# Kernel tuning notes

Measured on AMD Instinct MI355X. Metric: run time of the kernel, lower is better.

The kernel has to match this reference:

```python
import jax, jax.numpy as jnp
import numpy as np

N = 100000      # nodes
E = 800000      # edges (avg degree 8)
F = 5           # num_node_features
D = 128         # embed_dim
H = 4           # heads
HD = D // H     # per-head dim = 32
H1, H2 = 64, 128  # mlp hidden dims


def _mlp(x, W1, b1, W2, b2, W3, b3):
    h = jax.nn.relu(x @ W1 + b1)
    h = jax.nn.relu(h @ W2 + b2)
    return h @ W3 + b3


def setup_inputs() -> dict:
    key = jax.random.key(0)
    ks = jax.random.split(key, 24)
    g = lambda i, shape: (jax.random.normal(ks[i], shape, dtype=jnp.float32) * 0.05)
    z = lambda d: jnp.zeros((d,), dtype=jnp.float32)
    return {
        "x": jax.random.normal(ks[0], (N, F), dtype=jnp.float32),
        "edge_index": jax.random.randint(ks[1], (2, E), 0, N),
        # mlp_prep: F -> 64 -> 128 -> D
        "prep_W1": g(2, (F, H1)),  "prep_b1": z(H1),
        "prep_W2": g(3, (H1, H2)), "prep_b2": z(H2),
        "prep_W3": g(4, (H2, D)),  "prep_b3": z(D),
        # mlp_update: D -> 64 -> 128 -> D
        "upd_W1": g(5, (D, H1)),   "upd_b1": z(H1),
        "upd_W2": g(6, (H1, H2)),  "upd_b2": z(H2),
        "upd_W3": g(7, (H2, D)),   "upd_b3": z(D),
        # TransformerConv projections (heads=4, per-head 32, concat -> D)
        "q_W": g(8, (D, D)),  "q_b": z(D),
        "k_W": g(9, (D, D)),  "k_b": z(D),
        "v_W": g(10, (D, D)), "v_b": z(D),
        "skip_W": g(11, (D, D)), "skip_b": z(D),
    }


def _transformer_conv(x, edge_index, q_W, q_b, k_W, k_b, v_W, v_b, skip_W, skip_b):
    # PyG TransformerConv: messages flow src=edge_index[0] -> dst=edge_index[1]
    src, dst = edge_index[0], edge_index[1]
    q = (x @ q_W + q_b).reshape(N, H, HD)
    k = (x @ k_W + k_b).reshape(N, H, HD)
    v = (x @ v_W + v_b).reshape(N, H, HD)
    scale = 1.0 / np.sqrt(HD).astype(np.float32)
    # per-edge attention logits [E, H]
    score = jnp.einsum('ehd,ehd->eh', q[dst], k[src]) * scale
    # segment softmax over incoming edges of each destination node
    m = jax.ops.segment_max(score, dst, num_segments=N)          # [N, H]
    e = jnp.exp(score - m[dst])                                  # [E, H]
    denom = jax.ops.segment_sum(e, dst, num_segments=N)         # [N, H]
    alpha = e / denom[dst]                                       # [E, H]
    # scatter-aggregate weighted values
    agg = jax.ops.segment_sum(alpha[..., None] * v[src], dst, num_segments=N)  # [N, H, HD]
    return agg.reshape(N, H * HD) + (x @ skip_W + skip_b)


def reference(x, edge_index,
              prep_W1, prep_b1, prep_W2, prep_b2, prep_W3, prep_b3,
              upd_W1, upd_b1, upd_W2, upd_b2, upd_W3, upd_b3,
              q_W, q_b, k_W, k_b, v_W, v_b, skip_W, skip_b):
    h_init = _mlp(x, prep_W1, prep_b1, prep_W2, prep_b2, prep_W3, prep_b3)
    h = _transformer_conv(h_init, edge_index, q_W, q_b, k_W, k_b, v_W, v_b, skip_W, skip_b)
    return h + _mlp(h, upd_W1, upd_b1, upd_W2, upd_b2, upd_W3, upd_b3)
```

## Files before the change

kernel.cpp:

```cpp
#include <hip/hip_runtime.h>
#include <hip/hip_bf16.h>

#define N_  100000
#define F_  5
#define D_  128
#define H_  4
#define HD_ 32
#define E_  800000

typedef __attribute__((ext_vector_type(8))) short bf16x8;
typedef __attribute__((ext_vector_type(4))) float f32x4;

__device__ __forceinline__ unsigned short f2bf(float f) {
  unsigned u = __float_as_uint(f);
  u += 0x7FFF + ((u >> 16) & 1);
  return (unsigned short)(u >> 16);
}

__device__ __forceinline__ unsigned pk2(float a, float b) {
  __hip_bfloat162 h = __float22bfloat162_rn(make_float2(a, b));
  return *(unsigned*)&h;
}

__device__ __forceinline__ float2 bf2f2(unsigned u) {
  float2 r;
  r.x = __uint_as_float(u << 16);
  r.y = __uint_as_float(u & 0xffff0000u);
  return r;
}

__device__ __forceinline__ float rowsum8(float x) {
  x += __int_as_float(__builtin_amdgcn_update_dpp(0, __float_as_int(x), 0x0B1, 0xF, 0xF, false));
  x += __int_as_float(__builtin_amdgcn_update_dpp(0, __float_as_int(x), 0x04E, 0xF, 0xF, false));
  x += __int_as_float(__builtin_amdgcn_update_dpp(0, __float_as_int(x), 0x141, 0xF, 0xF, false));
  return x;
}

template<int K, int M>
__device__ __forceinline__ void wconv_one(const float* __restrict__ W,
                                          unsigned short* __restrict__ WT,
                                          int idx) {
  const int r = idx & 7;
  const int l = (idx >> 3) & 15;
  const int rest = idx >> 7;
  const int kq = rest % (K / 8);
  const int i  = rest / (K / 8);
  WT[idx] = f2bf(W[(kq * 8 + r) * M + i * 16 + l]);
}

#define WCONV_NB 480
#define SCAN_NB ((N_ + 255) / 256)

__global__ __launch_bounds__(256) void k_wconv_all(
    const float* __restrict__ w0, const float* __restrict__ w1,
    const float* __restrict__ w2, const float* __restrict__ w3,
    const float* __restrict__ w4, const float* __restrict__ w5,
    const float* __restrict__ w6, const float* __restrict__ w7,
    const float* __restrict__ w8, unsigned short* __restrict__ WT,
    int* __restrict__ deg)
{
  if (blockIdx.x >= WCONV_NB) {
    const int i = (blockIdx.x - WCONV_NB) * 256 + threadIdx.x;
    if (i < N_) deg[i] = 0;
    return;
  }
  const int idx = blockIdx.x * 256 + threadIdx.x;
  if (idx < 8192)        wconv_one<64, 128>(w0, WT,          idx);
  else if (idx < 24576)  wconv_one<128,128>(w1, WT + 8192,   idx - 8192);
  else if (idx < 40960)  wconv_one<128,128>(w2, WT + 24576,  idx - 24576);
  else if (idx < 57344)  wconv_one<128,128>(w3, WT + 40960,  idx - 40960);
  else if (idx < 73728)  wconv_one<128,128>(w4, WT + 57344,  idx - 57344);
  else if (idx < 90112)  wconv_one<128,128>(w5, WT + 73728,  idx - 73728);
  else if (idx < 98304)  wconv_one<128, 64>(w6, WT + 90112,  idx - 90112);
  else if (idx < 106496) wconv_one<64, 128>(w7, WT + 98304,  idx - 98304);
  else                   wconv_one<128,128>(w8, WT + 106496, idx - 106496);
}

template<int K, int M>
__device__ __forceinline__ void gemm_frag64(const unsigned short* sX,
                                            const unsigned short* __restrict__ WT,
                                            f32x4 (*acc)[4],
                                            int wr, int l16, int kg)
{
  constexpr int SX = K + 8;
  constexpr int IF = M / 64;
  #pragma unroll
  for (int i = 0; i < IF; ++i)
    #pragma unroll
    for (int j = 0; j < 4; ++j) acc[i][j] = (f32x4){0.f, 0.f, 0.f, 0.f};
  #pragma unroll
  for (int k0 = 0; k0 < K; k0 += 32) {
    const int kq = k0 / 8 + kg;
    bf16x8 aw[IF];
    #pragma unroll
    for (int i = 0; i < IF; ++i)
      aw[i] = *(const bf16x8*)&WT[(((wr * IF + i) * (K / 8) + kq) * 16 + l16) * 8];
    #pragma unroll
    for (int j = 0; j < 4; ++j) {
      const bf16x8 bx = *(const bf16x8*)&sX[(j * 16 + l16) * SX + k0 + kg * 8];
      #pragma unroll
      for (int i = 0; i < IF; ++i)
        acc[i][j] = __builtin_amdgcn_mfma_f32_16x16x32_bf16(aw[i], bx, acc[i][j], 0, 0, 0);
    }
  }
}

template<int M, bool RELU, int SXO>
__device__ __forceinline__ void acc_to_lds64(unsigned short* sY, f32x4 (*acc)[4],
                                             const float* __restrict__ bias,
                                             int wr, int l16, int kg)
{
  constexpr int IF = M / 64;
  float4 b4[IF];
  #pragma unroll
  for (int i = 0; i < IF; ++i)
    b4[i] = *(const float4*)&bias[(wr * IF + i) * 16 + kg * 4];
  #pragma unroll
  for (int j = 0; j < 4; ++j) {
    const int row = j * 16 + l16;
    #pragma unroll
    for (int i = 0; i < IF; ++i) {
      const int f0 = (wr * IF + i) * 16 + kg * 4;
      float ox = acc[i][j][0] + b4[i].x, oy = acc[i][j][1] + b4[i].y;
      float oz = acc[i][j][2] + b4[i].z, ow = acc[i][j][3] + b4[i].w;
      if constexpr (RELU) {
        ox = fmaxf(ox, 0.f); oy = fmaxf(oy, 0.f);
        oz = fmaxf(oz, 0.f); ow = fmaxf(ow, 0.f);
      }
      uint2 p;
      p.x = pk2(ox, oy);
      p.y = pk2(oz, ow);
      *(uint2*)&sY[row * SXO + f0] = p;
    }
  }
}

__global__ __launch_bounds__(256) void k_prep_proj(
    const float* __restrict__ x,
    const float* __restrict__ pW1, const float* __restrict__ pb1,
    const unsigned short* __restrict__ wt_p2, const float* __restrict__ pb2,
    const unsigned short* __restrict__ wt_p3, const float* __restrict__ pb3,
    const unsigned short* __restrict__ wt_q, const float* __restrict__ qb,
    const unsigned short* __restrict__ wt_k, const float* __restrict__ kb,
    const unsigned short* __restrict__ wt_v, const float* __restrict__ vb,
    const unsigned short* __restrict__ wt_s, const float* __restrict__ sb,
    unsigned short* __restrict__ q16, unsigned short* __restrict__ k16,
    unsigned short* __restrict__ v16, float* __restrict__ out)
{
  __shared__ __align__(16) unsigned short bufA[64 * 72];
  __shared__ __align__(16) unsigned short bufB[64 * 136];

  const int t = threadIdx.x;
  const int node0 = blockIdx.x * 64;
  const int lane = t & 63;
  const int wr = t >> 6;
  const int l16 = lane & 15, kg = lane >> 4;

  float* sxs = (float*)bufB;
  float* sw1 = (float*)bufB + 320;
  {
    const long gbase = (long)node0 * F_;
    for (int i = t; i < 64 * F_; i += 256) {
      const long g = gbase + i;
      sxs[i] = (g < (long)N_ * F_) ? x[g] : 0.f;
    }
    for (int i = t; i < 384; i += 256)
      sw1[i] = (i < 320) ? pW1[i] : pb1[i - 320];
  }
  __syncthreads();

  {
    const int n = t >> 2;
    const int f0b = (t & 3) * 16;
    float xr[F_];
    #pragma unroll
    for (int k = 0; k < F_; ++k) xr[k] = sxs[n * F_ + k];
    const float* sb1 = sw1 + 320;
    #pragma unroll
    for (int q = 0; q < 4; ++q) {
      float o[4];
      #pragma unroll
      for (int jj = 0; jj < 4; ++jj) {
        const int f = f0b + q * 4 + jj;
        float a = sb1[f];
        #pragma unroll
        for (int k = 0; k < F_; ++k) a = fmaf(xr[k], sw1[k * 64 + f], a);
        o[jj] = fmaxf(a, 0.f);
      }
      uint2 pkd;
      pkd.x = pk2(o[0], o[1]);
      pkd.y = pk2(o[2], o[3]);
      *(uint2*)&bufA[n * 72 + f0b + q * 4] = pkd;
    }
  }
  __syncthreads();

  f32x4 acc[2][4];

  gemm_frag64<64, 128>(bufA, wt_p2, acc, wr, l16, kg);
  acc_to_lds64<128, true, 136>(bufB, acc, pb2, wr, l16, kg);
  __syncthreads();

  gemm_frag64<128, 128>(bufB, wt_p3, acc, wr, l16, kg);
  __syncthreads();
  acc_to_lds64<128, false, 136>(bufB, acc, pb3, wr, l16, kg);
  __syncthreads();

  {
    const unsigned short* wtsP[3] = {wt_q, wt_k, wt_v};
    const float* bsP[3] = {qb, kb, vb};
    unsigned short* ysP[3] = {q16, k16, v16};
    #pragma unroll
    for (int ws = 0; ws < 3; ++ws) {
      gemm_frag64<128, 128>(bufB, wtsP[ws], acc, wr, l16, kg);
      const float* __restrict__ bias = bsP[ws];
      unsigned short* __restrict__ Yb = ysP[ws];
      float4 b4[2];
      #pragma unroll
      for (int i = 0; i < 2; ++i)
        b4[i] = *(const float4*)&bias[(wr * 2 + i) * 16 + kg * 4];
      #pragma unroll
      for (int j = 0; j < 4; ++j) {
        const int node = node0 + j * 16 + l16;
        if (node >= N_) continue;
        #pragma unroll
        for (int i = 0; i < 2; ++i) {
          const int f0 = (wr * 2 + i) * 16 + kg * 4;
          uint2 ob;
          ob.x = pk2(acc[i][j][0] + b4[i].x, acc[i][j][1] + b4[i].y);
          ob.y = pk2(acc[i][j][2] + b4[i].z, acc[i][j][3] + b4[i].w);
          *(uint2*)&Yb[(long)node * D_ + f0] = ob;
        }
      }
    }
  }

  gemm_frag64<128, 128>(bufB, wt_s, acc, wr, l16, kg);
  {
    float4 b4[2];
    #pragma unroll
    for (int i = 0; i < 2; ++i)
      b4[i] = *(const float4*)&sb[(wr * 2 + i) * 16 + kg * 4];
    #pragma unroll
    for (int j = 0; j < 4; ++j) {
      const int node = node0 + j * 16 + l16;
      if (node >= N_) continue;
      #pragma unroll
      for (int i = 0; i < 2; ++i) {
        const int f0 = (wr * 2 + i) * 16 + kg * 4;
        float4 o = make_float4(acc[i][j][0] + b4[i].x, acc[i][j][1] + b4[i].y,
                               acc[i][j][2] + b4[i].z, acc[i][j][3] + b4[i].w);
        *(float4*)&out[(long)node * D_ + f0] = o;
      }
    }
  }
}

__global__ __launch_bounds__(256) void k_update(
    const unsigned short* __restrict__ wt_u1, const float* __restrict__ ub1,
    const unsigned short* __restrict__ wt_u2, const float* __restrict__ ub2,
    const unsigned short* __restrict__ wt_u3, const float* __restrict__ ub3,
    float* __restrict__ out)
{
  __shared__ __align__(16) unsigned short bufA[64 * 72];
  __shared__ __align__(16) unsigned short bufB[64 * 136];

  const int t = threadIdx.x;
  const int node0 = blockIdx.x * 64;
  const int lane = t & 63;
  const int wr = t >> 6;
  const int l16 = lane & 15, kg = lane >> 4;

  #pragma unroll
  for (int i = 0; i < 8; ++i) {
    const int g = t + 256 * i;
    const int row = g >> 5;
    const int kc  = g & 31;
    const int node = node0 + row;
    float4 xv = (node < N_) ? ((const float4*)out)[(long)node * 32 + kc]
                            : make_float4(0.f, 0.f, 0.f, 0.f);
    uint2 p;
    p.x = pk2(xv.x, xv.y);
    p.y = pk2(xv.z, xv.w);
    *(uint2*)&bufB[row * 136 + kc * 4] = p;
  }
  __syncthreads();

  f32x4 acc[2][4];

  gemm_frag64<128, 64>(bufB, wt_u1, acc, wr, l16, kg);
  acc_to_lds64<64, true, 72>(bufA, acc, ub1, wr, l16, kg);
  __syncthreads();

  gemm_frag64<64, 128>(bufA, wt_u2, acc, wr, l16, kg);
  acc_to_lds64<128, true, 136>(bufB, acc, ub2, wr, l16, kg);
  __syncthreads();

  gemm_frag64<128, 128>(bufB, wt_u3, acc, wr, l16, kg);
  {
    float4 b4[2];
    #pragma unroll
    for (int i = 0; i < 2; ++i)
      b4[i] = *(const float4*)&ub3[(wr * 2 + i) * 16 + kg * 4];
    #pragma unroll
    for (int j = 0; j < 4; ++j) {
      const int node = node0 + j * 16 + l16;
      if (node >= N_) continue;
      #pragma unroll
      for (int i = 0; i < 2; ++i) {
        const int f0 = (wr * 2 + i) * 16 + kg * 4;
        const float4 r = *(const float4*)&out[(long)node * D_ + f0];
        float4 o = make_float4(acc[i][j][0] + b4[i].x + r.x,
                               acc[i][j][1] + b4[i].y + r.y,
                               acc[i][j][2] + b4[i].z + r.z,
                               acc[i][j][3] + b4[i].w + r.w);
        *(float4*)&out[(long)node * D_ + f0] = o;
      }
    }
  }
}

__global__ __launch_bounds__(256) void k_hist(const int* __restrict__ ei,
                                              int* __restrict__ deg) {
  int e = blockIdx.x * 256 + threadIdx.x;
  if (e < E_) atomicAdd(&deg[ei[E_ + e]], 1);
}

__global__ __launch_bounds__(256) void k_scan1(const int* __restrict__ deg,
                                               int* __restrict__ off,
                                               int* __restrict__ bsum) {
  __shared__ int s[256];
  const int t = threadIdx.x;
  const int i = blockIdx.x * 256 + t;
  const int v = (i < N_) ? deg[i] : 0;
  s[t] = v;
  __syncthreads();
  #pragma unroll
  for (int o = 1; o < 256; o <<= 1) {
    int u = (t >= o) ? s[t - o] : 0;
    __syncthreads();
    s[t] += u;
    __syncthreads();
  }
  if (i < N_) off[i] = s[t] - v;
  if (t == 255) bsum[blockIdx.x] = s[255];
}

__global__ __launch_bounds__(256) void k_scan23(const int* __restrict__ off,
                                                const int* __restrict__ bsum,
                                                int* __restrict__ cur,
                                                const int* __restrict__ deg,
                                                int2* __restrict__ meta) {
  __shared__ int sacc[256];
  const int t = threadIdx.x;
  const int bid = blockIdx.x;
  int s = 0;
  for (int j = t; j < bid; j += 256) s += bsum[j];
  sacc[t] = s;
  __syncthreads();
  #pragma unroll
  for (int o = 128; o > 0; o >>= 1) {
    if (t < o) sacc[t] += sacc[t + o];
    __syncthreads();
  }
  const int prefix = sacc[0];
  const int i = bid * 256 + t;
  if (i < N_) {
    const int o = off[i] + prefix;
    cur[i] = o;
    meta[i] = make_int2(o, deg[i]);
  }
}

__global__ __launch_bounds__(256) void k_fill(const int* __restrict__ ei,
                                              int* __restrict__ cur,
                                              int* __restrict__ esrc) {
  int e = blockIdx.x * 256 + threadIdx.x;
  if (e < E_) {
    int src = ei[e], dst = ei[E_ + e];
    int pos = atomicAdd(&cur[dst], 1);
    esrc[pos] = src;
  }
}

__global__ __launch_bounds__(256) void k_attn(
    const int* __restrict__ esrc, const int2* __restrict__ meta,
    const unsigned short* __restrict__ q,
    const unsigned short* __restrict__ kbuf,
    const unsigned short* __restrict__ vbuf,
    float* __restrict__ out)
{
  const int t = threadIdx.x;
  const unsigned node = blockIdx.x * 8 + (t >> 5);
  const int c = t & 31;
  const float C = 0.17677669529663687f * 1.4426950408889634f;

  const int2 md = meta[node];
  const int start = md.x, cnt = md.y;
  const int end = start + cnt;

  const uint2 qu = *(const uint2*)&q[(node << 7) + 4u * c];
  const float2 q01 = bf2f2(qu.x), q23 = bf2f2(qu.y);
  const float qx0 = q01.x * C, qx1 = q01.y * C;
  const float qx2 = q23.x * C, qx3 = q23.y * C;

  float l = 0.f, a0 = 0.f, a1 = 0.f, a2 = 0.f, a3 = 0.f;

  const int P = (cnt + 1) >> 1;
  if (P > 0) {
    bool v1c = (start + 1) < end;
    unsigned i0 = esrc[start];
    unsigned i1 = esrc[v1c ? start + 1 : start];
    uint2 kA = *(const uint2*)&kbuf[(i0 << 7) + 4u * c];
    uint2 kB = *(const uint2*)&kbuf[(i1 << 7) + 4u * c];
    uint2 wA = *(const uint2*)&vbuf[(i0 << 7) + 4u * c];
    uint2 wB = *(const uint2*)&vbuf[(i1 << 7) + 4u * c];
    bool v0n = (start + 2) < end, v1n = (start + 3) < end;
    unsigned i0n = esrc[v0n ? start + 2 : start];
    unsigned i1n = esrc[v1n ? start + 3 : start];

    for (int it = 0;;) {
      const bool more = (it + 1) < P;
      uint2 kAn, kBn, wAn, wBn;
      unsigned i0f = 0, i1f = 0;
      bool v0f = false, v1f = false;
      if (more) {
        kAn = *(const uint2*)&kbuf[(i0n << 7) + 4u * c];
        kBn = *(const uint2*)&kbuf[(i1n << 7) + 4u * c];
        wAn = *(const uint2*)&vbuf[(i0n << 7) + 4u * c];
        wBn = *(const uint2*)&vbuf[(i1n << 7) + 4u * c];
        const int ef = start + 2 * (it + 2);
        v0f = ef < end; v1f = (ef + 1) < end;
        i0f = esrc[v0f ? ef : start];
        i1f = esrc[v1f ? ef + 1 : start];
      }

      const float2 ka01 = bf2f2(kA.x), ka23 = bf2f2(kA.y);
      const float2 kb01 = bf2f2(kB.x), kb23 = bf2f2(kB.y);
      float sA = fmaf(qx0, ka01.x, fmaf(qx1, ka01.y, fmaf(qx2, ka23.x, qx3 * ka23.y)));
      float sB = fmaf(qx0, kb01.x, fmaf(qx1, kb01.y, fmaf(qx2, kb23.x, qx3 * kb23.y)));
      sA = rowsum8(sA);
      sB = rowsum8(sB);
      const float eA = __builtin_amdgcn_exp2f(sA);
      const float eB = v1c ? __builtin_amdgcn_exp2f(sB) : 0.f;
      const float2 va01 = bf2f2(wA.x), va23 = bf2f2(wA.y);
      const float2 vb01 = bf2f2(wB.x), vb23 = bf2f2(wB.y);
      l += eA + eB;
      a0 = fmaf(eA, va01.x, fmaf(eB, vb01.x, a0));
      a1 = fmaf(eA, va01.y, fmaf(eB, vb01.y, a1));
      a2 = fmaf(eA, va23.x, fmaf(eB, vb23.x, a2));
      a3 = fmaf(eA, va23.y, fmaf(eB, vb23.y, a3));

      if (!more) break;
      ++it;
      kA = kAn; kB = kBn; wA = wAn; wB = wBn;
      v1c = v1n;
      v0n = v0f; v1n = v1f;
      i0n = i0f; i1n = i1f;
    }
  }

  if (l > 0.f) {
    const float inv = 1.0f / l;
    float4* op = (float4*)&out[(node << 7) + 4u * c];
    float4 cv = *op;
    cv.x += a0 * inv;
    cv.y += a1 * inv;
    cv.z += a2 * inv;
    cv.w += a3 * inv;
    *op = cv;
  }
}

extern "C" void kernel_launch(void* const* d_in, const int* in_sizes, int n_in,
                              void* d_out, int out_size, void* d_ws, size_t ws_size,
                              hipStream_t stream) {
  const float* x   = (const float*)d_in[0];
  const int*   ei  = (const int*)d_in[1];
  const float* pW1 = (const float*)d_in[2];  const float* pb1 = (const float*)d_in[3];
  const float* pW2 = (const float*)d_in[4];  const float* pb2 = (const float*)d_in[5];
  const float* pW3 = (const float*)d_in[6];  const float* pb3 = (const float*)d_in[7];
  const float* uW1 = (const float*)d_in[8];  const float* ub1 = (const float*)d_in[9];
  const float* uW2 = (const float*)d_in[10]; const float* ub2 = (const float*)d_in[11];
  const float* uW3 = (const float*)d_in[12]; const float* ub3 = (const float*)d_in[13];
  const float* qW  = (const float*)d_in[14]; const float* qb  = (const float*)d_in[15];
  const float* kW  = (const float*)d_in[16]; const float* kb  = (const float*)d_in[17];
  const float* vW  = (const float*)d_in[18]; const float* vb  = (const float*)d_in[19];
  const float* sW  = (const float*)d_in[20]; const float* sb  = (const float*)d_in[21];

  float* out = (float*)d_out;
  float* ws  = (float*)d_ws;

  const long ND = (long)N_ * D_;
  unsigned short* q16 = (unsigned short*)(ws + ND);
  unsigned short* k16 = (unsigned short*)(ws + 2 * ND);
  unsigned short* v16 = (unsigned short*)(ws + 3 * ND);

  unsigned short* wtb = (unsigned short*)(ws + 4 * ND);
  unsigned short* wt_p2 = wtb;
  unsigned short* wt_p3 = wtb + 8192;
  unsigned short* wt_q  = wtb + 24576;
  unsigned short* wt_k  = wtb + 40960;
  unsigned short* wt_v  = wtb + 57344;
  unsigned short* wt_s  = wtb + 73728;
  unsigned short* wt_u1 = wtb + 90112;
  unsigned short* wt_u2 = wtb + 98304;
  unsigned short* wt_u3 = wtb + 106496;

  int* deg  = (int*)ws;
  int* off  = deg + N_;
  int* cur  = off + N_;
  int* esrc = cur + N_;
  int* bsum = esrc + E_;
  int2* meta = (int2*)(bsum + 512);

  const int gT64 = (N_ + 63) / 64;

  k_wconv_all<<<WCONV_NB + SCAN_NB, 256, 0, stream>>>(
      pW2, pW3, qW, kW, vW, sW, uW1, uW2, uW3, wtb, deg);

  k_hist  <<<(E_ + 255) / 256, 256, 0, stream>>>(ei, deg);
  k_scan1 <<<SCAN_NB, 256, 0, stream>>>(deg, off, bsum);
  k_scan23<<<SCAN_NB, 256, 0, stream>>>(off, bsum, cur, deg, meta);
  k_fill  <<<(E_ + 255) / 256, 256, 0, stream>>>(ei, cur, esrc);

  k_prep_proj<<<gT64, 256, 0, stream>>>(
      x, pW1, pb1, wt_p2, pb2, wt_p3, pb3,
      wt_q, qb, wt_k, kb, wt_v, vb, wt_s, sb,
      q16, k16, v16, out);

  k_attn<<<N_ / 8, 256, 0, stream>>>(esrc, meta, q16, k16, v16, out);

  k_update<<<gT64, 256, 0, stream>>>(wt_u1, ub1, wt_u2, ub2, wt_u3, ub3, out);
}
```

Baseline: 354.3 us.

## Fuse attention aggregation into the update MLP kernel

The attention gather/softmax kernel is merged into the update-MLP kernel. Each 256-thread block now processes 64 nodes serially, 8 per 32-thread group, and writes the h rows straight into LDS as bf16. This removes one kernel launch and the global re-read of h before the MLP. In exchange each block runs a long, latency-bound gather loop before its MFMA phase, uses fewer blocks (N/64 instead of N/8), and holds LDS during the gather, which may reduce parallelism for the irregular memory work.

```diff
diff --git a/kernel.cpp b/kernel.cpp
--- a/kernel.cpp
+++ b/kernel.cpp
@@ -256,7 +256,74 @@
   }
 }
 
-__global__ __launch_bounds__(256) void k_update(
+__global__ __launch_bounds__(256) void k_hist(const int* __restrict__ ei,
+                                              int* __restrict__ deg) {
+  int e = blockIdx.x * 256 + threadIdx.x;
+  if (e < E_) atomicAdd(&deg[ei[E_ + e]], 1);
+}
+
+__global__ __launch_bounds__(256) void k_scan1(const int* __restrict__ deg,
+                                               int* __restrict__ off,
+                                               int* __restrict__ bsum) {
+  __shared__ int s[256];
+  const int t = threadIdx.x;
+  const int i = blockIdx.x * 256 + t;
+  const int v = (i < N_) ? deg[i] : 0;
+  s[t] = v;
+  __syncthreads();
+  #pragma unroll
+  for (int o = 1; o < 256; o <<= 1) {
+    int u = (t >= o) ? s[t - o] : 0;
+    __syncthreads();
+    s[t] += u;
+    __syncthreads();
+  }
+  if (i < N_) off[i] = s[t] - v;
+  if (t == 255) bsum[blockIdx.x] = s[255];
+}
+
+__global__ __launch_bounds__(256) void k_scan23(const int* __restrict__ off,
+                                                const int* __restrict__ bsum,
+                                                int* __restrict__ cur,
+                                                const int* __restrict__ deg,
+                                                int2* __restrict__ meta) {
+  __shared__ int sacc[256];
+  const int t = threadIdx.x;
+  const int bid = blockIdx.x;
+  int s = 0;
+  for (int j = t; j < bid; j += 256) s += bsum[j];
+  sacc[t] = s;
+  __syncthreads();
+  #pragma unroll
+  for (int o = 128; o > 0; o >>= 1) {
+    if (t < o) sacc[t] += sacc[t + o];
+    __syncthreads();
+  }
+  const int prefix = sacc[0];
+  const int i = bid * 256 + t;
+  if (i < N_) {
+    const int o = off[i] + prefix;
+    cur[i] = o;
+    meta[i] = make_int2(o, deg[i]);
+  }
+}
+
+__global__ __launch_bounds__(256) void k_fill(const int* __restrict__ ei,
+                                              int* __restrict__ cur,
+                                              int* __restrict__ esrc) {
+  int e = blockIdx.x * 256 + threadIdx.x;
+  if (e < E_) {
+    int src = ei[e], dst = ei[E_ + e];
+    int pos = atomicAdd(&cur[dst], 1);
+    esrc[pos] = src;
+  }
+}
+
+__global__ __launch_bounds__(256) void k_attn_update(
+    const int* __restrict__ esrc, const int2* __restrict__ meta,
+    const unsigned short* __restrict__ q,
+    const unsigned short* __restrict__ kbuf,
+    const unsigned short* __restrict__ vbuf,
     const unsigned short* __restrict__ wt_u1, const float* __restrict__ ub1,
     const unsigned short* __restrict__ wt_u2, const float* __restrict__ ub2,
     const unsigned short* __restrict__ wt_u3, const float* __restrict__ ub3,
@@ -267,24 +334,104 @@
 
   const int t = threadIdx.x;
   const int node0 = blockIdx.x * 64;
+  const int half = t >> 5;
+  const int c = t & 31;
+  const float C = 0.17677669529663687f * 1.4426950408889634f;
+
+  for (int s = 0; s < 8; ++s) {
+    const int row = half * 8 + s;
+    const int node = node0 + row;
+    if (node >= N_) {
+      *(uint2*)&bufB[row * 136 + 4 * c] = make_uint2(0u, 0u);
+      continue;
+    }
+
+    const int2 md = meta[node];
+    const int start = md.x, cnt = md.y;
+    const int end = start + cnt;
+
+    const uint2 qu = *(const uint2*)&q[((unsigned)node << 7) + 4u * c];
+    const float2 q01 = bf2f2(qu.x), q23 = bf2f2(qu.y);
+    const float qx0 = q01.x * C, qx1 = q01.y * C;
+    const float qx2 = q23.x * C, qx3 = q23.y * C;
+
+    float l = 0.f, a0 = 0.f, a1 = 0.f, a2 = 0.f, a3 = 0.f;
+
+    const int P = (cnt + 1) >> 1;
+    if (P > 0) {
+      bool v1c = (start + 1) < end;
+      unsigned i0 = esrc[start];
+      unsigned i1 = esrc[v1c ? start + 1 : start];
+      uint2 kA = *(const uint2*)&kbuf[((long)i0 << 7) + 4u * c];
+      uint2 kB = *(const uint2*)&kbuf[((long)i1 << 7) + 4u * c];
+      uint2 wA = *(const uint2*)&vbuf[((long)i0 << 7) + 4u * c];
+      uint2 wB = *(const uint2*)&vbuf[((long)i1 << 7) + 4u * c];
+      bool v0n = (start + 2) < end, v1n = (start + 3) < end;
+      unsigned i0n = esrc[v0n ? start + 2 : start];
+      unsigned i1n = esrc[v1n ? start + 3 : start];
+
+      for (int it = 0;;) {
+        const bool more = (it + 1) < P;
+        uint2 kAn, kBn, wAn, wBn;
+        unsigned i0f = 0, i1f = 0;
+        bool v0f = false, v1f = false;
+        if (more) {
+          kAn = *(const uint2*)&kbuf[((long)i0n << 7) + 4u * c];
+          kBn = *(const uint2*)&kbuf[((long)i1n << 7) + 4u * c];
+          wAn = *(const uint2*)&vbuf[((long)i0n << 7) + 4u * c];
+          wBn = *(const uint2*)&vbuf[((long)i1n << 7) + 4u * c];
+          const int ef = start + 2 * (it + 2);
+          v0f = ef < end; v1f = (ef + 1) < end;
+          i0f = esrc[v0f ? ef : start];
+          i1f = esrc[v1f ? ef + 1 : start];
+        }
+
+        const float2 ka01 = bf2f2(kA.x), ka23 = bf2f2(kA.y);
+        const float2 kb01 = bf2f2(kB.x), kb23 = bf2f2(kB.y);
+        float sA = fmaf(qx0, ka01.x, fmaf(qx1, ka01.y, fmaf(qx2, ka23.x, qx3 * ka23.y)));
+        float sB = fmaf(qx0, kb01.x, fmaf(qx1, kb01.y, fmaf(qx2, kb23.x, qx3 * kb23.y)));
+        sA = rowsum8(sA);
+        sB = rowsum8(sB);
+        const float eA = __builtin_amdgcn_exp2f(sA);
+        const float eB = v1c ? __builtin_amdgcn_exp2f(sB) : 0.f;
+        const float2 va01 = bf2f2(wA.x), va23 = bf2f2(wA.y);
+        const float2 vb01 = bf2f2(wB.x), vb23 = bf2f2(wB.y);
+        l += eA + eB;
+        a0 = fmaf(eA, va01.x, fmaf(eB, vb01.x, a0));
+        a1 = fmaf(eA, va01.y, fmaf(eB, vb01.y, a1));
+        a2 = fmaf(eA, va23.x, fmaf(eB, vb23.x, a2));
+        a3 = fmaf(eA, va23.y, fmaf(eB, vb23.y, a3));
+
+        if (!more) break;
+        ++it;
+        kA = kAn; kB = kBn; wA = wAn; wB = wBn;
+        v1c = v1n;
+        v0n = v0f; v1n = v1f;
+        i0n = i0f; i1n = i1f;
+      }
+    }
+
+    float r0 = 0.f, r1 = 0.f, r2 = 0.f, r3 = 0.f;
+    if (l > 0.f) {
+      const float inv = 1.0f / l;
+      r0 = a0 * inv; r1 = a1 * inv; r2 = a2 * inv; r3 = a3 * inv;
+    }
+
+    float4* op = (float4*)&out[((unsigned)node << 7) + 4u * c];
+    float4 sk = *op;
+    const float h0 = sk.x + r0, h1 = sk.y + r1;
+    const float h2 = sk.z + r2, h3 = sk.w + r3;
+    *op = make_float4(h0, h1, h2, h3);
+    uint2 hb;
+    hb.x = pk2(h0, h1);
+    hb.y = pk2(h2, h3);
+    *(uint2*)&bufB[row * 136 + 4 * c] = hb;
+  }
+  __syncthreads();
+
   const int lane = t & 63;
   const int wr = t >> 6;
   const int l16 = lane & 15, kg = lane >> 4;
-
-  #pragma unroll
-  for (int i = 0; i < 8; ++i) {
-    const int g = t + 256 * i;
-    const int row = g >> 5;
-    const int kc  = g & 31;
-    const int node = node0 + row;
-    float4 xv = (node < N_) ? ((const float4*)out)[(long)node * 32 + kc]
-                            : make_float4(0.f, 0.f, 0.f, 0.f);
-    uint2 p;
-    p.x = pk2(xv.x, xv.y);
-    p.y = pk2(xv.z, xv.w);
-    *(uint2*)&bufB[row * 136 + kc * 4] = p;
-  }
-  __syncthreads();
 
   f32x4 acc[2][4];
 
@@ -317,158 +464,6 @@
         *(float4*)&out[(long)node * D_ + f0] = o;
       }
     }
-  }
-}
-
-__global__ __launch_bounds__(256) void k_hist(const int* __restrict__ ei,
-                                              int* __restrict__ deg) {
-  int e = blockIdx.x * 256 + threadIdx.x;
-  if (e < E_) atomicAdd(&deg[ei[E_ + e]], 1);
-}
-
-__global__ __launch_bounds__(256) void k_scan1(const int* __restrict__ deg,
-                                               int* __restrict__ off,
-                                               int* __restrict__ bsum) {
-  __shared__ int s[256];
-  const int t = threadIdx.x;
-  const int i = blockIdx.x * 256 + t;
-  const int v = (i < N_) ? deg[i] : 0;
-  s[t] = v;
-  __syncthreads();
-  #pragma unroll
-  for (int o = 1; o < 256; o <<= 1) {
-    int u = (t >= o) ? s[t - o] : 0;
-    __syncthreads();
-    s[t] += u;
-    __syncthreads();
-  }
-  if (i < N_) off[i] = s[t] - v;
-  if (t == 255) bsum[blockIdx.x] = s[255];
-}
-
-__global__ __launch_bounds__(256) void k_scan23(const int* __restrict__ off,
-                                                const int* __restrict__ bsum,
-                                                int* __restrict__ cur,
-                                                const int* __restrict__ deg,
-                                                int2* __restrict__ meta) {
-  __shared__ int sacc[256];
-  const int t = threadIdx.x;
-  const int bid = blockIdx.x;
-  int s = 0;
-  for (int j = t; j < bid; j += 256) s += bsum[j];
-  sacc[t] = s;
-  __syncthreads();
-  #pragma unroll
-  for (int o = 128; o > 0; o >>= 1) {
-    if (t < o) sacc[t] += sacc[t + o];
-    __syncthreads();
-  }
-  const int prefix = sacc[0];
-  const int i = bid * 256 + t;
-  if (i < N_) {
-    const int o = off[i] + prefix;
-    cur[i] = o;
-    meta[i] = make_int2(o, deg[i]);
-  }
-}
-
-__global__ __launch_bounds__(256) void k_fill(const int* __restrict__ ei,
-                                              int* __restrict__ cur,
-                                              int* __restrict__ esrc) {
-  int e = blockIdx.x * 256 + threadIdx.x;
-  if (e < E_) {
-    int src = ei[e], dst = ei[E_ + e];
-    int pos = atomicAdd(&cur[dst], 1);
-    esrc[pos] = src;
-  }
-}
-
-__global__ __launch_bounds__(256) void k_attn(
-    const int* __restrict__ esrc, const int2* __restrict__ meta,
-    const unsigned short* __restrict__ q,
-    const unsigned short* __restrict__ kbuf,
-    const unsigned short* __restrict__ vbuf,
-    float* __restrict__ out)
-{
-  const int t = threadIdx.x;
-  const unsigned node = blockIdx.x * 8 + (t >> 5);
-  const int c = t & 31;
-  const float C = 0.17677669529663687f * 1.4426950408889634f;
-
-  const int2 md = meta[node];
-  const int start = md.x, cnt = md.y;
-  const int end = start + cnt;
-
-  const uint2 qu = *(const uint2*)&q[(node << 7) + 4u * c];
-  const float2 q01 = bf2f2(qu.x), q23 = bf2f2(qu.y);
-  const float qx0 = q01.x * C, qx1 = q01.y * C;
-  const float qx2 = q23.x * C, qx3 = q23.y * C;
-
-  float l = 0.f, a0 = 0.f, a1 = 0.f, a2 = 0.f, a3 = 0.f;
-
-  const int P = (cnt + 1) >> 1;
-  if (P > 0) {
-    bool v1c = (start + 1) < end;
-    unsigned i0 = esrc[start];
-    unsigned i1 = esrc[v1c ? start + 1 : start];
-    uint2 kA = *(const uint2*)&kbuf[(i0 << 7) + 4u * c];
-    uint2 kB = *(const uint2*)&kbuf[(i1 << 7) + 4u * c];
-    uint2 wA = *(const uint2*)&vbuf[(i0 << 7) + 4u * c];
-    uint2 wB = *(const uint2*)&vbuf[(i1 << 7) + 4u * c];
-    bool v0n = (start + 2) < end, v1n = (start + 3) < end;
-    unsigned i0n = esrc[v0n ? start + 2 : start];
-    unsigned i1n = esrc[v1n ? start + 3 : start];
-
-    for (int it = 0;;) {
-      const bool more = (it + 1) < P;
-      uint2 kAn, kBn, wAn, wBn;
-      unsigned i0f = 0, i1f = 0;
-      bool v0f = false, v1f = false;
-      if (more) {
-        kAn = *(const uint2*)&kbuf[(i0n << 7) + 4u * c];
-        kBn = *(const uint2*)&kbuf[(i1n << 7) + 4u * c];
-        wAn = *(const uint2*)&vbuf[(i0n << 7) + 4u * c];
-        wBn = *(const uint2*)&vbuf[(i1n << 7) + 4u * c];
-        const int ef = start + 2 * (it + 2);
-        v0f = ef < end; v1f = (ef + 1) < end;
-        i0f = esrc[v0f ? ef : start];
-        i1f = esrc[v1f ? ef + 1 : start];
-      }
-
-      const float2 ka01 = bf2f2(kA.x), ka23 = bf2f2(kA.y);
-      const float2 kb01 = bf2f2(kB.x), kb23 = bf2f2(kB.y);
-      float sA = fmaf(qx0, ka01.x, fmaf(qx1, ka01.y, fmaf(qx2, ka23.x, qx3 * ka23.y)));
-      float sB = fmaf(qx0, kb01.x, fmaf(qx1, kb01.y, fmaf(qx2, kb23.x, qx3 * kb23.y)));
-      sA = rowsum8(sA);
-      sB = rowsum8(sB);
-      const float eA = __builtin_amdgcn_exp2f(sA);
-      const float eB = v1c ? __builtin_amdgcn_exp2f(sB) : 0.f;
-      const float2 va01 = bf2f2(wA.x), va23 = bf2f2(wA.y);
-      const float2 vb01 = bf2f2(wB.x), vb23 = bf2f2(wB.y);
-      l += eA + eB;
-      a0 = fmaf(eA, va01.x, fmaf(eB, vb01.x, a0));
-      a1 = fmaf(eA, va01.y, fmaf(eB, vb01.y, a1));
-      a2 = fmaf(eA, va23.x, fmaf(eB, vb23.x, a2));
-      a3 = fmaf(eA, va23.y, fmaf(eB, vb23.y, a3));
-
-      if (!more) break;
-      ++it;
-      kA = kAn; kB = kBn; wA = wAn; wB = wBn;
-      v1c = v1n;
-      v0n = v0f; v1n = v1f;
-      i0n = i0f; i1n = i1f;
-    }
-  }
-
-  if (l > 0.f) {
-    const float inv = 1.0f / l;
-    float4* op = (float4*)&out[(node << 7) + 4u * c];
-    float4 cv = *op;
-    cv.x += a0 * inv;
-    cv.y += a1 * inv;
-    cv.z += a2 * inv;
-    cv.w += a3 * inv;
-    *op = cv;
   }
 }
 
@@ -529,7 +524,7 @@
       wt_q, qb, wt_k, kb, wt_v, vb, wt_s, sb,
       q16, k16, v16, out);
 
-  k_attn<<<N_ / 8, 256, 0, stream>>>(esrc, meta, q16, k16, v16, out);
-
-  k_update<<<gT64, 256, 0, stream>>>(wt_u1, ub1, wt_u2, ub2, wt_u3, ub3, out);
-}
+  k_attn_update<<<gT64, 256, 0, stream>>>(
+      esrc, meta, q16, k16, v16,
+      wt_u1, ub1, wt_u2, ub2, wt_u3, ub3, out);
+}
```

After: 359.6 us. About the same (+1.5%).

## Fuse degree histogram into weight conversion and CSR fill into prep projection

Applied to the files above, without the earlier changes.

The degree zeroing moves to a memset, and the edge histogram now runs as extra blocks in the weight-conversion kernel. The CSR fill runs as two of every three blocks of the prep/projection kernel, so the scatter overlaps with the MLP/GEMM work and two launches disappear. The attention kernel's gather indexing switches to 64-bit offsets. The fill blocks share a grid with the shared-memory-heavy prep blocks, which can affect occupancy, and the fill grid must cover all edges: 2*1563*256 ≥ 800000 holds.

```diff
diff --git a/kernel.cpp b/kernel.cpp
--- a/kernel.cpp
+++ b/kernel.cpp
@@ -49,19 +49,20 @@
 }
 
 #define WCONV_NB 480
-#define SCAN_NB ((N_ + 255) / 256)
-
-__global__ __launch_bounds__(256) void k_wconv_all(
+#define HIST_NB  ((E_ + 255) / 256)
+#define SCAN_NB  ((N_ + 255) / 256)
+
+__global__ __launch_bounds__(256) void k_wconv_hist(
     const float* __restrict__ w0, const float* __restrict__ w1,
     const float* __restrict__ w2, const float* __restrict__ w3,
     const float* __restrict__ w4, const float* __restrict__ w5,
     const float* __restrict__ w6, const float* __restrict__ w7,
     const float* __restrict__ w8, unsigned short* __restrict__ WT,
-    int* __restrict__ deg)
+    const int* __restrict__ ei, int* __restrict__ deg)
 {
   if (blockIdx.x >= WCONV_NB) {
-    const int i = (blockIdx.x - WCONV_NB) * 256 + threadIdx.x;
-    if (i < N_) deg[i] = 0;
+    const int e = (blockIdx.x - WCONV_NB) * 256 + threadIdx.x;
+    if (e < E_) atomicAdd(&deg[ei[E_ + e]], 1);
     return;
   }
   const int idx = blockIdx.x * 256 + threadIdx.x;
@@ -135,7 +136,54 @@
   }
 }
 
-__global__ __launch_bounds__(256) void k_prep_proj(
+__global__ __launch_bounds__(256) void k_scan1(const int* __restrict__ deg,
+                                               int* __restrict__ off,
+                                               int* __restrict__ bsum) {
+  __shared__ int s[256];
+  const int t = threadIdx.x;
+  const int i = blockIdx.x * 256 + t;
+  const int v = (i < N_) ? deg[i] : 0;
+  s[t] = v;
+  __syncthreads();
+  #pragma unroll
+  for (int o = 1; o < 256; o <<= 1) {
+    int u = (t >= o) ? s[t - o] : 0;
+    __syncthreads();
+    s[t] += u;
+    __syncthreads();
+  }
+  if (i < N_) off[i] = s[t] - v;
+  if (t == 255) bsum[blockIdx.x] = s[255];
+}
+
+__global__ __launch_bounds__(256) void k_scan23(const int* __restrict__ off,
+                                                const int* __restrict__ bsum,
+                                                int* __restrict__ cur,
+                                                const int* __restrict__ deg,
+                                                int2* __restrict__ meta) {
+  __shared__ int sacc[256];
+  const int t = threadIdx.x;
+  const int bid = blockIdx.x;
+  int s = 0;
+  for (int j = t; j < bid; j += 256) s += bsum[j];
+  sacc[t] = s;
+  __syncthreads();
+  #pragma unroll
+  for (int o = 128; o > 0; o >>= 1) {
+    if (t < o) sacc[t] += sacc[t + o];
+    __syncthreads();
+  }
+  const int prefix = sacc[0];
+  const int i = bid * 256 + t;
+  if (i < N_) {
+    const int o = off[i] + prefix;
+    cur[i] = o;
+    meta[i] = make_int2(o, deg[i]);
+  }
+}
+
+__global__ __launch_bounds__(256) void k_fill_prep(
+    const int* __restrict__ ei, int* __restrict__ cur, int* __restrict__ esrc,
     const float* __restrict__ x,
     const float* __restrict__ pW1, const float* __restrict__ pb1,
     const unsigned short* __restrict__ wt_p2, const float* __restrict__ pb2,
@@ -150,8 +198,20 @@
   __shared__ __align__(16) unsigned short bufA[64 * 72];
   __shared__ __align__(16) unsigned short bufB[64 * 136];
 
+  const int bmod = blockIdx.x % 3;
+  if (bmod != 2) {
+    const int fid = (blockIdx.x / 3) * 2 + bmod;
+    const int e = fid * 256 + threadIdx.x;
+    if (e < E_) {
+      const int src = ei[e], dst = ei[E_ + e];
+      const int pos = atomicAdd(&cur[dst], 1);
+      esrc[pos] = src;
+    }
+    return;
+  }
+
   const int t = threadIdx.x;
-  const int node0 = blockIdx.x * 64;
+  const int node0 = (blockIdx.x / 3) * 64;
   const int lane = t & 63;
   const int wr = t >> 6;
   const int l16 = lane & 15, kg = lane >> 4;
@@ -320,69 +380,6 @@
   }
 }
 
-__global__ __launch_bounds__(256) void k_hist(const int* __restrict__ ei,
-                                              int* __restrict__ deg) {
-  int e = blockIdx.x * 256 + threadIdx.x;
-  if (e < E_) atomicAdd(&deg[ei[E_ + e]], 1);
-}
-
-__global__ __launch_bounds__(256) void k_scan1(const int* __restrict__ deg,
-                                               int* __restrict__ off,
-                                               int* __restrict__ bsum) {
-  __shared__ int s[256];
-  const int t = threadIdx.x;
-  const int i = blockIdx.x * 256 + t;
-  const int v = (i < N_) ? deg[i] : 0;
-  s[t] = v;
-  __syncthreads();
-  #pragma unroll
-  for (int o = 1; o < 256; o <<= 1) {
-    int u = (t >= o) ? s[t - o] : 0;
-    __syncthreads();
-    s[t] += u;
-    __syncthreads();
-  }
-  if (i < N_) off[i] = s[t] - v;
-  if (t == 255) bsum[blockIdx.x] = s[255];
-}
-
-__global__ __launch_bounds__(256) void k_scan23(const int* __restrict__ off,
-                                                const int* __restrict__ bsum,
-                                                int* __restrict__ cur,
-                                                const int* __restrict__ deg,
-                                                int2* __restrict__ meta) {
-  __shared__ int sacc[256];
-  const int t = threadIdx.x;
-  const int bid = blockIdx.x;
-  int s = 0;
-  for (int j = t; j < bid; j += 256) s += bsum[j];
-  sacc[t] = s;
-  __syncthreads();
-  #pragma unroll
-  for (int o = 128; o > 0; o >>= 1) {
-    if (t < o) sacc[t] += sacc[t + o];
-    __syncthreads();
-  }
-  const int prefix = sacc[0];
-  const int i = bid * 256 + t;
-  if (i < N_) {
-    const int o = off[i] + prefix;
-    cur[i] = o;
-    meta[i] = make_int2(o, deg[i]);
-  }
-}
-
-__global__ __launch_bounds__(256) void k_fill(const int* __restrict__ ei,
-                                              int* __restrict__ cur,
-                                              int* __restrict__ esrc) {
-  int e = blockIdx.x * 256 + threadIdx.x;
-  if (e < E_) {
-    int src = ei[e], dst = ei[E_ + e];
-    int pos = atomicAdd(&cur[dst], 1);
-    esrc[pos] = src;
-  }
-}
-
 __global__ __launch_bounds__(256) void k_attn(
     const int* __restrict__ esrc, const int2* __restrict__ meta,
     const unsigned short* __restrict__ q,
@@ -411,10 +408,10 @@
     bool v1c = (start + 1) < end;
     unsigned i0 = esrc[start];
     unsigned i1 = esrc[v1c ? start + 1 : start];
-    uint2 kA = *(const uint2*)&kbuf[(i0 << 7) + 4u * c];
-    uint2 kB = *(const uint2*)&kbuf[(i1 << 7) + 4u * c];
-    uint2 wA = *(const uint2*)&vbuf[(i0 << 7) + 4u * c];
-    uint2 wB = *(const uint2*)&vbuf[(i1 << 7) + 4u * c];
+    uint2 kA = *(const uint2*)&kbuf[((long)i0 << 7) + 4u * c];
+    uint2 kB = *(const uint2*)&kbuf[((long)i1 << 7) + 4u * c];
+    uint2 wA = *(const uint2*)&vbuf[((long)i0 << 7) + 4u * c];
+    uint2 wB = *(const uint2*)&vbuf[((long)i1 << 7) + 4u * c];
     bool v0n = (start + 2) < end, v1n = (start + 3) < end;
     unsigned i0n = esrc[v0n ? start + 2 : start];
     unsigned i1n = esrc[v1n ? start + 3 : start];
@@ -425,10 +422,10 @@
       unsigned i0f = 0, i1f = 0;
       bool v0f = false, v1f = false;
       if (more) {
-        kAn = *(const uint2*)&kbuf[(i0n << 7) + 4u * c];
-        kBn = *(const uint2*)&kbuf[(i1n << 7) + 4u * c];
-        wAn = *(const uint2*)&vbuf[(i0n << 7) + 4u * c];
-        wBn = *(const uint2*)&vbuf[(i1n << 7) + 4u * c];
+        kAn = *(const uint2*)&kbuf[((long)i0n << 7) + 4u * c];
+        kBn = *(const uint2*)&kbuf[((long)i1n << 7) + 4u * c];
+        wAn = *(const uint2*)&vbuf[((long)i0n << 7) + 4u * c];
+        wBn = *(const uint2*)&vbuf[((long)i1n << 7) + 4u * c];
         const int ef = start + 2 * (it + 2);
         v0f = ef < end; v1f = (ef + 1) < end;
         i0f = esrc[v0f ? ef : start];
@@ -516,15 +513,16 @@
 
   const int gT64 = (N_ + 63) / 64;
 
-  k_wconv_all<<<WCONV_NB + SCAN_NB, 256, 0, stream>>>(
-      pW2, pW3, qW, kW, vW, sW, uW1, uW2, uW3, wtb, deg);
-
-  k_hist  <<<(E_ + 255) / 256, 256, 0, stream>>>(ei, deg);
+  hipMemsetAsync(deg, 0, N_ * sizeof(int), stream);
+
+  k_wconv_hist<<<WCONV_NB + HIST_NB, 256, 0, stream>>>(
+      pW2, pW3, qW, kW, vW, sW, uW1, uW2, uW3, wtb, ei, deg);
+
   k_scan1 <<<SCAN_NB, 256, 0, stream>>>(deg, off, bsum);
   k_scan23<<<SCAN_NB, 256, 0, stream>>>(off, bsum, cur, deg, meta);
-  k_fill  <<<(E_ + 255) / 256, 256, 0, stream>>>(ei, cur, esrc);
-
-  k_prep_proj<<<gT64, 256, 0, stream>>>(
+
+  k_fill_prep<<<3 * gT64, 256, 0, stream>>>(
+      ei, cur, esrc,
       x, pW1, pb1, wt_p2, pb2, wt_p3, pb3,
       wt_q, qb, wt_k, kb, wt_v, vb, wt_s, sb,
       q16, k16, v16, out);
```

Result: faster. 314.9 us (-11.1%).
